# Kernel optimization log

Hardware: AMD Instinct MI355X
Metric: run time of the kernel (lower is better)

The kernel has to match this reference:

```python
import jax, jax.numpy as jnp
import numpy as np

BN_EPS = 1e-5


def setup_inputs() -> dict:
    key = jax.random.key(0)
    k1, k2, k3, k4 = jax.random.split(key, 4)
    N_IN, N_OUT, K, M, C_IN, C_OUT = 500000, 125000, 27, 60000, 64, 64
    x = jax.random.normal(k1, (N_IN, C_IN), dtype=jnp.float32)
    # Per-offset conv weights, fan-in scaled like Minkowski's kaiming init
    W = jax.random.normal(k2, (K, C_IN, C_OUT), dtype=jnp.float32) * (1.0 / np.sqrt(K * C_IN))
    gamma = jnp.ones((C_OUT,), dtype=jnp.float32)
    beta = jnp.zeros((C_OUT,), dtype=jnp.float32)
    # Kernel map: for each of the 27 offsets, M (input_idx, output_idx) pairs
    in_idx = jax.random.randint(k3, (K, M), 0, N_IN, dtype=jnp.int64)
    out_idx = jax.random.randint(k4, (K, M), 0, N_OUT, dtype=jnp.int64)
    return {"x": x, "W": W, "gamma": gamma, "beta": beta,
            "in_idx": in_idx, "out_idx": out_idx, "n_out": 125000}


def reference(x, W, gamma, beta, in_idx, out_idx, n_out):
    # Sparse 3D conv via kernel map: gather -> per-offset GEMM -> scatter-add.
    C_out = W.shape[-1]
    gathered = x[in_idx]                                   # [K, M, C_in]
    contrib = jnp.einsum('kmc,kcd->kmd', gathered, W)      # [K, M, C_out]
    out = jnp.zeros((n_out, C_out), dtype=x.dtype)
    out = out.at[out_idx.reshape(-1)].add(contrib.reshape(-1, C_out))  # [N_out, C_out]
    # MinkowskiBatchNorm (training mode): per-channel batch stats over all points
    mean = jnp.mean(out, axis=0)
    var = jnp.mean(jnp.square(out - mean), axis=0)         # biased variance
    y = (out - mean) * jax.lax.rsqrt(var + BN_EPS) * gamma + beta
    return y
```

## Files before the change

### kernel.cpp

```cpp
#include <hip/hip_runtime.h>

typedef __attribute__((ext_vector_type(8))) short short8;
typedef __attribute__((ext_vector_type(4))) float f32x4;

#define K_OFF    27
#define M_PAIRS  60000
#define C_DIM    64
#define N_IN     500000
#define N_OUT_C  125000
#define BN_EPS   1e-5f
#define E_TOT    (K_OFF * M_PAIRS)

#define TILE_ROWS    32
#define TILES_PER_K  (M_PAIRS / TILE_ROWS)
#define TOTAL_WT     (K_OFF * TILES_PER_K)

#define CONTRIB_BYTES ((size_t)E_TOT * C_DIM * 2)
#define WT_OFF    CONTRIB_BYTES
#define WT_BYTES  ((size_t)K_OFF * C_DIM * C_DIM * 2)
#define CNT_OFF   (WT_OFF + WT_BYTES)
#define CNT_BYTES ((size_t)N_OUT_C * 4)
#define OFF_OFF   (CNT_OFF + CNT_BYTES)
#define CUR_OFF   (OFF_OFF + CNT_BYTES)
#define BSUM_OFF  (CUR_OFF + CNT_BYTES)
#define ST_OFF    (BSUM_OFF + 4096)
#define XB_OFF    ((ST_OFF + 512 + 255) & ~(size_t)255)
#define XB_BYTES  ((size_t)N_IN * C_DIM * 2)
#define WS_MID    XB_OFF
#define WS_FULL   (XB_OFF + XB_BYTES)

#define SCAN_BS 256
#define SCAN_NB ((N_OUT_C + SCAN_BS - 1) / SCAN_BS)

#define PREP_XBLK 2048
#define PREP_WBLK ((K_OFF * C_DIM * C_DIM + 255) / 256)
#define PREP_HBLK 1024

__device__ __forceinline__ unsigned short f32_to_bf16(float f) {
    unsigned u = __float_as_uint(f);
    u += 0x7FFFu + ((u >> 16) & 1u);
    return (unsigned short)(u >> 16);
}
__device__ __forceinline__ float bf16f(unsigned short u) {
    return __uint_as_float((unsigned)u << 16);
}

__global__ __launch_bounds__(256) void prep(
    const float* __restrict__ x, unsigned short* __restrict__ xb,
    const float* __restrict__ W, unsigned short* __restrict__ wt,
    const int* __restrict__ out_idx, unsigned* __restrict__ cnt, int nx)
{
    int b = blockIdx.x;
    if (b < nx) {
        const int tid = b * 256 + threadIdx.x;
        const int T   = nx * 256;
        const int n4  = N_IN * C_DIM / 4;
        const float4* x4 = (const float4*)x;
        ushort4* b4 = (ushort4*)xb;
        for (int i = tid; i < n4; i += T) {
            float4 v = x4[i];
            ushort4 o;
            o.x = f32_to_bf16(v.x); o.y = f32_to_bf16(v.y);
            o.z = f32_to_bf16(v.z); o.w = f32_to_bf16(v.w);
            b4[i] = o;
        }
        return;
    }
    b -= nx;
    if (b < PREP_WBLK) {
        const int tid = b * 256 + threadIdx.x;
        if (tid < K_OFF * C_DIM * C_DIM) {
            const int c = tid & 63;
            const int d = (tid >> 6) & 63;
            const int k = tid >> 12;
            wt[tid] = f32_to_bf16(W[(k << 12) + (c << 6) + d]);
        }
        return;
    }
    b -= PREP_WBLK;
    for (int e = b * 256 + threadIdx.x; e < E_TOT; e += PREP_HBLK * 256)
        atomicAdd(&cnt[out_idx[e]], 1u);
}

__global__ __launch_bounds__(SCAN_BS) void scan_a(const unsigned* __restrict__ cnt,
                                                  unsigned* __restrict__ off,
                                                  unsigned* __restrict__ bsum) {
    __shared__ unsigned s[SCAN_BS];
    const int idx = blockIdx.x * SCAN_BS + threadIdx.x;
    const unsigned v = (idx < N_OUT_C) ? cnt[idx] : 0u;
    s[threadIdx.x] = v;
    __syncthreads();
    for (int d = 1; d < SCAN_BS; d <<= 1) {
        unsigned t = (threadIdx.x >= d) ? s[threadIdx.x - d] : 0u;
        __syncthreads();
        s[threadIdx.x] += t;
        __syncthreads();
    }
    if (idx < N_OUT_C) off[idx] = s[threadIdx.x] - v;
    if (threadIdx.x == SCAN_BS - 1) bsum[blockIdx.x] = s[threadIdx.x];
}

__global__ __launch_bounds__(512) void scan_b(unsigned* __restrict__ bsum) {
    __shared__ unsigned s[512];
    const unsigned v = (threadIdx.x < SCAN_NB) ? bsum[threadIdx.x] : 0u;
    s[threadIdx.x] = v;
    __syncthreads();
    for (int d = 1; d < 512; d <<= 1) {
        unsigned t = (threadIdx.x >= d) ? s[threadIdx.x - d] : 0u;
        __syncthreads();
        s[threadIdx.x] += t;
        __syncthreads();
    }
    if (threadIdx.x < SCAN_NB) bsum[threadIdx.x] = s[threadIdx.x] - v;
}

__global__ __launch_bounds__(SCAN_BS) void scan_c(unsigned* __restrict__ off,
                                                  unsigned* __restrict__ cur,
                                                  const unsigned* __restrict__ bsum) {
    const int idx = blockIdx.x * SCAN_BS + threadIdx.x;
    if (idx < N_OUT_C) {
        const unsigned o = off[idx] + bsum[blockIdx.x];
        off[idx] = o;
        cur[idx] = o;
    }
}

template<bool BF16G>
__global__ __launch_bounds__(256, 5) void mfma_contrib(
    const float* __restrict__ x, const unsigned short* __restrict__ xb,
    const unsigned short* __restrict__ wt,
    const int* __restrict__ in_idx, const int* __restrict__ out_idx,
    unsigned* __restrict__ cursor, unsigned short* __restrict__ contrib)
{
    const int gwave = blockIdx.x * 4 + (threadIdx.x >> 6);
    if (gwave >= TOTAL_WT) return;
    const int lane = threadIdx.x & 63;
    const int lg = lane >> 4;
    const int lr = lane & 15;

    const int k  = gwave / TILES_PER_K;
    const int t  = gwave % TILES_PER_K;
    const int m0 = t * TILE_ROWS;
    const int kbase = k * M_PAIRS;

    short8 bfr[2][4];
    const unsigned short* wtk = wt + (size_t)k * C_DIM * C_DIM;
#pragma unroll
    for (int ks = 0; ks < 2; ++ks)
#pragma unroll
        for (int ct = 0; ct < 4; ++ct)
            bfr[ks][ct] = *(const short8*)(wtk + (ct * 16 + lr) * C_DIM + ks * 32 + lg * 8);

    int pos = 0;
    if (lane < TILE_ROWS)
        pos = (int)atomicAdd(&cursor[out_idx[kbase + m0 + lane]], 1u);

    int aidx[2];
#pragma unroll
    for (int rt = 0; rt < 2; ++rt)
        aidx[rt] = in_idx[kbase + m0 + rt * 16 + lr];

    f32x4 acc[2][4] = {};
#pragma unroll
    for (int ks = 0; ks < 2; ++ks) {
#pragma unroll
        for (int rt = 0; rt < 2; ++rt) {
            short8 a;
            if constexpr (BF16G) {
                a = *(const short8*)(xb + (size_t)aidx[rt] * C_DIM + ks * 32 + lg * 8);
            } else {
                const float* xr = x + (size_t)aidx[rt] * C_DIM + ks * 32 + lg * 8;
                float4 f0 = *(const float4*)xr;
                float4 f1 = *(const float4*)(xr + 4);
                a[0] = (short)f32_to_bf16(f0.x); a[1] = (short)f32_to_bf16(f0.y);
                a[2] = (short)f32_to_bf16(f0.z); a[3] = (short)f32_to_bf16(f0.w);
                a[4] = (short)f32_to_bf16(f1.x); a[5] = (short)f32_to_bf16(f1.y);
                a[6] = (short)f32_to_bf16(f1.z); a[7] = (short)f32_to_bf16(f1.w);
            }
#pragma unroll
            for (int ct = 0; ct < 4; ++ct)
                acc[rt][ct] = __builtin_amdgcn_mfma_f32_16x16x32_bf16(
                    a, bfr[ks][ct], acc[rt][ct], 0, 0, 0);
        }
    }

#pragma unroll
    for (int rt = 0; rt < 2; ++rt) {
#pragma unroll
        for (int j = 0; j < 4; ++j) {
            const int r = rt * 16 + lg * 4 + j;
            const int p = __shfl(pos, r);
#pragma unroll
            for (int ct = 0; ct < 4; ++ct) {
                const float v0 = acc[rt][ct][j];
                const float v1 = __shfl_xor(v0, 1);
                if ((lane & 1) == 0) {
                    const unsigned pk = (unsigned)f32_to_bf16(v0)
                                      | ((unsigned)f32_to_bf16(v1) << 16);
                    *(unsigned*)(contrib + (size_t)p * C_DIM + ct * 16 + lr) = pk;
                }
            }
        }
    }
}

__global__ __launch_bounds__(256) void reduce_bn(
    const unsigned short* __restrict__ contrib, const unsigned* __restrict__ off,
    const unsigned* __restrict__ cnt, float* __restrict__ out,
    float* __restrict__ stats)
{
    __shared__ float ls[128];
    if (threadIdx.x < 128) ls[threadIdx.x] = 0.f;
    __syncthreads();
    const int lane = threadIdx.x & 63;
    const int wid  = blockIdx.x * 4 + (threadIdx.x >> 6);
    const int NW   = gridDim.x * 4;
    const int span = (N_OUT_C + NW - 1) / NW;
    const int o0 = wid * span;
    const int o1 = (o0 + span < N_OUT_C) ? o0 + span : N_OUT_C;

    float ssum = 0.f, ssq = 0.f;
    for (int o = o0; o < o1; ++o) {
        const unsigned base = off[o];
        const unsigned n    = cnt[o];
        const unsigned short* p = contrib + (size_t)base * C_DIM + lane;
        float a0 = 0.f, a1 = 0.f, a2 = 0.f, a3 = 0.f;
        unsigned i = 0;
        for (; i + 4 <= n; i += 4) {
            a0 += bf16f(p[(size_t)(i + 0) * C_DIM]);
            a1 += bf16f(p[(size_t)(i + 1) * C_DIM]);
            a2 += bf16f(p[(size_t)(i + 2) * C_DIM]);
            a3 += bf16f(p[(size_t)(i + 3) * C_DIM]);
        }
        for (; i < n; ++i) a0 += bf16f(p[(size_t)i * C_DIM]);
        const float acc = (a0 + a1) + (a2 + a3);
        out[(size_t)o * C_DIM + lane] = acc;
        ssum += acc;
        ssq = fmaf(acc, acc, ssq);
    }
    atomicAdd(&ls[lane], ssum);
    atomicAdd(&ls[64 + lane], ssq);
    __syncthreads();
    if (threadIdx.x < 128) unsafeAtomicAdd(&stats[threadIdx.x], ls[threadIdx.x]);
}

__global__ __launch_bounds__(256) void bn_apply_f32(
    float* __restrict__ out, const float* __restrict__ stats,
    const float* __restrict__ gamma, const float* __restrict__ beta)
{
    __shared__ float ssc[C_DIM], ssh[C_DIM];
    if (threadIdx.x < C_DIM) {
        const float inv_n = 1.0f / (float)N_OUT_C;
        float mean = stats[threadIdx.x] * inv_n;
        float var  = stats[C_DIM + threadIdx.x] * inv_n - mean * mean;
        float inv  = rsqrtf(var + BN_EPS);
        float s    = inv * gamma[threadIdx.x];
        ssc[threadIdx.x] = s;
        ssh[threadIdx.x] = beta[threadIdx.x] - mean * s;
    }
    __syncthreads();
    const int tid = blockIdx.x * blockDim.x + threadIdx.x;
    const int T   = gridDim.x * blockDim.x;
    const int cq  = (tid & 15) * 4;
    const int total4 = N_OUT_C * C_DIM / 4;
    const float4 sc = make_float4(ssc[cq], ssc[cq+1], ssc[cq+2], ssc[cq+3]);
    const float4 sh = make_float4(ssh[cq], ssh[cq+1], ssh[cq+2], ssh[cq+3]);
    float4* o4 = (float4*)out;
    for (int i = tid; i < total4; i += T) {
        float4 v = o4[i];
        v.x = fmaf(v.x, sc.x, sh.x);
        v.y = fmaf(v.y, sc.y, sh.y);
        v.z = fmaf(v.z, sc.z, sh.z);
        v.w = fmaf(v.w, sc.w, sh.w);
        o4[i] = v;
    }
}

#define FCHUNKS  37
#define FWPK     (FCHUNKS * 4)
#define FSPAN    ((M_PAIRS + FWPK - 1) / FWPK)

__global__ __launch_bounds__(256, 4) void conv_scatter(
    const float* __restrict__ x, const float* __restrict__ W,
    const int* __restrict__ in_idx, const int* __restrict__ out_idx,
    float* __restrict__ out)
{
    const int k     = blockIdx.x / FCHUNKS;
    const int chunk = blockIdx.x % FCHUNKS;
    const int wid   = chunk * 4 + (threadIdx.x >> 6);
    const int lane  = threadIdx.x & 63;
    float wcol[C_DIM];
    const float* Wk = W + (size_t)k * C_DIM * C_DIM;
#pragma unroll
    for (int c = 0; c < C_DIM; ++c) wcol[c] = Wk[c * C_DIM + lane];
    const int kbase = k * M_PAIRS;
    const int m0 = wid * FSPAN;
    const int m1 = (m0 + FSPAN < M_PAIRS) ? m0 + FSPAN : M_PAIRS;
    for (int m = m0; m < m1; ++m) {
        int ii = __builtin_amdgcn_readfirstlane(in_idx[kbase + m]);
        int oi = __builtin_amdgcn_readfirstlane(out_idx[kbase + m]);
        const float* xr = x + (size_t)ii * C_DIM;
        float a0=0.f,a1=0.f,a2=0.f,a3=0.f;
#pragma unroll
        for (int c = 0; c < C_DIM; c += 4) {
            a0 = fmaf(xr[c+0], wcol[c+0], a0);
            a1 = fmaf(xr[c+1], wcol[c+1], a1);
            a2 = fmaf(xr[c+2], wcol[c+2], a2);
            a3 = fmaf(xr[c+3], wcol[c+3], a3);
        }
        unsafeAtomicAdd(out + (size_t)oi * C_DIM + lane, (a0+a1)+(a2+a3));
    }
}

__global__ __launch_bounds__(256) void bn_stats_f32(
    const float* __restrict__ acc, float* __restrict__ stats)
{
    const int tid = blockIdx.x * blockDim.x + threadIdx.x;
    const int T   = gridDim.x * blockDim.x;
    const int cq  = (tid & 15) * 4;
    const int total4 = N_OUT_C * C_DIM / 4;
    float s0=0,s1=0,s2=0,s3=0,q0=0,q1=0,q2=0,q3=0;
    const float4* a4 = (const float4*)acc;
    for (int i = tid; i < total4; i += T) {
        float4 v = a4[i];
        s0+=v.x; q0=fmaf(v.x,v.x,q0);
        s1+=v.y; q1=fmaf(v.y,v.y,q1);
        s2+=v.z; q2=fmaf(v.z,v.z,q2);
        s3+=v.w; q3=fmaf(v.w,v.w,q3);
    }
    __shared__ float ls[128];
    if (threadIdx.x < 128) ls[threadIdx.x] = 0.f;
    __syncthreads();
    atomicAdd(&ls[cq+0],s0); atomicAdd(&ls[cq+1],s1);
    atomicAdd(&ls[cq+2],s2); atomicAdd(&ls[cq+3],s3);
    atomicAdd(&ls[64+cq+0],q0); atomicAdd(&ls[64+cq+1],q1);
    atomicAdd(&ls[64+cq+2],q2); atomicAdd(&ls[64+cq+3],q3);
    __syncthreads();
    if (threadIdx.x < 128) unsafeAtomicAdd(&stats[threadIdx.x], ls[threadIdx.x]);
}

extern "C" void kernel_launch(void* const* d_in, const int* in_sizes, int n_in,
                              void* d_out, int out_size, void* d_ws, size_t ws_size,
                              hipStream_t stream)
{
    const float* x       = (const float*)d_in[0];
    const float* W       = (const float*)d_in[1];
    const float* gamma   = (const float*)d_in[2];
    const float* beta    = (const float*)d_in[3];
    const int*   in_idx  = (const int*)d_in[4];
    const int*   out_idx = (const int*)d_in[5];
    float* out = (float*)d_out;

    if (ws_size >= WS_MID) {
        unsigned short* contrib = (unsigned short*)d_ws;
        unsigned short* wt      = (unsigned short*)((char*)d_ws + WT_OFF);
        unsigned* cnt           = (unsigned*)((char*)d_ws + CNT_OFF);
        unsigned* off           = (unsigned*)((char*)d_ws + OFF_OFF);
        unsigned* cur           = (unsigned*)((char*)d_ws + CUR_OFF);
        unsigned* bsum          = (unsigned*)((char*)d_ws + BSUM_OFF);
        float* stats            = (float*)((char*)d_ws + ST_OFF);
        unsigned short* xb      = (unsigned short*)((char*)d_ws + XB_OFF);
        const bool full         = (ws_size >= WS_FULL);
        const int nx            = full ? PREP_XBLK : 0;

        hipMemsetAsync(cnt, 0, CNT_BYTES, stream);
        hipMemsetAsync(stats, 0, 128 * sizeof(float), stream);
        prep<<<nx + PREP_WBLK + PREP_HBLK, 256, 0, stream>>>(
            x, xb, W, wt, out_idx, cnt, nx);
        scan_a<<<SCAN_NB, SCAN_BS, 0, stream>>>(cnt, off, bsum);
        scan_b<<<1, 512, 0, stream>>>(bsum);
        scan_c<<<SCAN_NB, SCAN_BS, 0, stream>>>(off, cur, bsum);
        if (full)
            mfma_contrib<true><<<(TOTAL_WT + 3) / 4, 256, 0, stream>>>(
                x, xb, wt, in_idx, out_idx, cur, contrib);
        else
            mfma_contrib<false><<<(TOTAL_WT + 3) / 4, 256, 0, stream>>>(
                x, xb, wt, in_idx, out_idx, cur, contrib);
        reduce_bn<<<2048, 256, 0, stream>>>(contrib, off, cnt, out, stats);
        bn_apply_f32<<<1024, 256, 0, stream>>>(out, stats, gamma, beta);
    } else {
        float* stats = (float*)d_ws;
        hipMemsetAsync(out, 0, (size_t)N_OUT_C * C_DIM * sizeof(float), stream);
        hipMemsetAsync(stats, 0, 128 * sizeof(float), stream);
        conv_scatter<<<K_OFF * FCHUNKS, 256, 0, stream>>>(x, W, in_idx, out_idx, out);
        bn_stats_f32<<<512, 256, 0, stream>>>(out, stats);
        bn_apply_f32<<<1024, 256, 0, stream>>>(out, stats, gamma, beta);
    }
}
```

Baseline: 402.1 us.

## Enlarge MFMA contrib tiles to 64 rows and vectorize reduce_bn row loads

```diff
diff --git a/kernel.cpp b/kernel.cpp
--- a/kernel.cpp
+++ b/kernel.cpp
@@ -11,8 +11,7 @@
 #define BN_EPS   1e-5f
 #define E_TOT    (K_OFF * M_PAIRS)
 
-#define TILE_ROWS    32
-#define TILES_PER_K  (M_PAIRS / TILE_ROWS)
+#define TILES_PER_K  ((M_PAIRS + 63) / 64)
 #define TOTAL_WT     (K_OFF * TILES_PER_K)
 
 #define CONTRIB_BYTES ((size_t)E_TOT * C_DIM * 2)
@@ -126,7 +125,7 @@
 }
 
 template<bool BF16G>
-__global__ __launch_bounds__(256, 5) void mfma_contrib(
+__global__ __launch_bounds__(256, 4) void mfma_contrib(
     const float* __restrict__ x, const unsigned short* __restrict__ xb,
     const unsigned short* __restrict__ wt,
     const int* __restrict__ in_idx, const int* __restrict__ out_idx,
@@ -140,7 +139,7 @@
 
     const int k  = gwave / TILES_PER_K;
     const int t  = gwave % TILES_PER_K;
-    const int m0 = t * TILE_ROWS;
+    const int m0 = t * 64;
     const int kbase = k * M_PAIRS;
 
     short8 bfr[2][4];
@@ -151,31 +150,38 @@
         for (int ct = 0; ct < 4; ++ct)
             bfr[ks][ct] = *(const short8*)(wtk + (ct * 16 + lr) * C_DIM + ks * 32 + lg * 8);
 
-    int pos = 0;
-    if (lane < TILE_ROWS)
-        pos = (int)atomicAdd(&cursor[out_idx[kbase + m0 + lane]], 1u);
-
-    int aidx[2];
-#pragma unroll
-    for (int rt = 0; rt < 2; ++rt)
-        aidx[rt] = in_idx[kbase + m0 + rt * 16 + lr];
-
-    f32x4 acc[2][4] = {};
+    int pos = -1;
+    {
+        const int mrow = m0 + lane;
+        if (mrow < M_PAIRS)
+            pos = (int)atomicAdd(&cursor[out_idx[kbase + mrow]], 1u);
+    }
+
+    int aidx[4];
+#pragma unroll
+    for (int rt = 0; rt < 4; ++rt) {
+        const int m = m0 + rt * 16 + lr;
+        aidx[rt] = (m < M_PAIRS) ? in_idx[kbase + m] : -1;
+    }
+
+    f32x4 acc[4][4] = {};
 #pragma unroll
     for (int ks = 0; ks < 2; ++ks) {
 #pragma unroll
-        for (int rt = 0; rt < 2; ++rt) {
-            short8 a;
-            if constexpr (BF16G) {
-                a = *(const short8*)(xb + (size_t)aidx[rt] * C_DIM + ks * 32 + lg * 8);
-            } else {
-                const float* xr = x + (size_t)aidx[rt] * C_DIM + ks * 32 + lg * 8;
-                float4 f0 = *(const float4*)xr;
-                float4 f1 = *(const float4*)(xr + 4);
-                a[0] = (short)f32_to_bf16(f0.x); a[1] = (short)f32_to_bf16(f0.y);
-                a[2] = (short)f32_to_bf16(f0.z); a[3] = (short)f32_to_bf16(f0.w);
-                a[4] = (short)f32_to_bf16(f1.x); a[5] = (short)f32_to_bf16(f1.y);
-                a[6] = (short)f32_to_bf16(f1.z); a[7] = (short)f32_to_bf16(f1.w);
+        for (int rt = 0; rt < 4; ++rt) {
+            short8 a = {};
+            if (aidx[rt] >= 0) {
+                if constexpr (BF16G) {
+                    a = *(const short8*)(xb + (size_t)aidx[rt] * C_DIM + ks * 32 + lg * 8);
+                } else {
+                    const float* xr = x + (size_t)aidx[rt] * C_DIM + ks * 32 + lg * 8;
+                    float4 f0 = *(const float4*)xr;
+                    float4 f1 = *(const float4*)(xr + 4);
+                    a[0] = (short)f32_to_bf16(f0.x); a[1] = (short)f32_to_bf16(f0.y);
+                    a[2] = (short)f32_to_bf16(f0.z); a[3] = (short)f32_to_bf16(f0.w);
+                    a[4] = (short)f32_to_bf16(f1.x); a[5] = (short)f32_to_bf16(f1.y);
+                    a[6] = (short)f32_to_bf16(f1.z); a[7] = (short)f32_to_bf16(f1.w);
+                }
             }
 #pragma unroll
             for (int ct = 0; ct < 4; ++ct)
@@ -185,20 +191,16 @@
     }
 
 #pragma unroll
-    for (int rt = 0; rt < 2; ++rt) {
+    for (int rt = 0; rt < 4; ++rt) {
 #pragma unroll
         for (int j = 0; j < 4; ++j) {
             const int r = rt * 16 + lg * 4 + j;
             const int p = __shfl(pos, r);
-#pragma unroll
-            for (int ct = 0; ct < 4; ++ct) {
-                const float v0 = acc[rt][ct][j];
-                const float v1 = __shfl_xor(v0, 1);
-                if ((lane & 1) == 0) {
-                    const unsigned pk = (unsigned)f32_to_bf16(v0)
-                                      | ((unsigned)f32_to_bf16(v1) << 16);
-                    *(unsigned*)(contrib + (size_t)p * C_DIM + ct * 16 + lr) = pk;
-                }
+            if (p >= 0) {
+                unsigned short* dst = contrib + (size_t)p * C_DIM + lr;
+#pragma unroll
+                for (int ct = 0; ct < 4; ++ct)
+                    dst[ct * 16] = f32_to_bf16(acc[rt][ct][j]);
             }
         }
     }
@@ -213,33 +215,45 @@
     if (threadIdx.x < 128) ls[threadIdx.x] = 0.f;
     __syncthreads();
     const int lane = threadIdx.x & 63;
+    const int lg = lane >> 4;
+    const int lr = lane & 15;
     const int wid  = blockIdx.x * 4 + (threadIdx.x >> 6);
     const int NW   = gridDim.x * 4;
     const int span = (N_OUT_C + NW - 1) / NW;
     const int o0 = wid * span;
     const int o1 = (o0 + span < N_OUT_C) ? o0 + span : N_OUT_C;
 
-    float ssum = 0.f, ssq = 0.f;
+    float ts0 = 0, ts1 = 0, ts2 = 0, ts3 = 0;
+    float tq0 = 0, tq1 = 0, tq2 = 0, tq3 = 0;
     for (int o = o0; o < o1; ++o) {
         const unsigned base = off[o];
-        const unsigned n    = cnt[o];
-        const unsigned short* p = contrib + (size_t)base * C_DIM + lane;
-        float a0 = 0.f, a1 = 0.f, a2 = 0.f, a3 = 0.f;
-        unsigned i = 0;
-        for (; i + 4 <= n; i += 4) {
-            a0 += bf16f(p[(size_t)(i + 0) * C_DIM]);
-            a1 += bf16f(p[(size_t)(i + 1) * C_DIM]);
-            a2 += bf16f(p[(size_t)(i + 2) * C_DIM]);
-            a3 += bf16f(p[(size_t)(i + 3) * C_DIM]);
-        }
-        for (; i < n; ++i) a0 += bf16f(p[(size_t)i * C_DIM]);
-        const float acc = (a0 + a1) + (a2 + a3);
-        out[(size_t)o * C_DIM + lane] = acc;
-        ssum += acc;
-        ssq = fmaf(acc, acc, ssq);
-    }
-    atomicAdd(&ls[lane], ssum);
-    atomicAdd(&ls[64 + lane], ssq);
+        const int n = (int)cnt[o];
+        float s0 = 0, s1 = 0, s2 = 0, s3 = 0;
+        for (int i = lg; i < n; i += 4) {
+            const ushort4 u = *(const ushort4*)(
+                contrib + ((size_t)base + i) * C_DIM + lr * 4);
+            s0 += bf16f(u.x); s1 += bf16f(u.y);
+            s2 += bf16f(u.z); s3 += bf16f(u.w);
+        }
+        s0 += __shfl_xor(s0, 16); s1 += __shfl_xor(s1, 16);
+        s2 += __shfl_xor(s2, 16); s3 += __shfl_xor(s3, 16);
+        s0 += __shfl_xor(s0, 32); s1 += __shfl_xor(s1, 32);
+        s2 += __shfl_xor(s2, 32); s3 += __shfl_xor(s3, 32);
+        if (lg == 0) {
+            *(float4*)(out + (size_t)o * C_DIM + lr * 4) =
+                make_float4(s0, s1, s2, s3);
+            ts0 += s0; tq0 = fmaf(s0, s0, tq0);
+            ts1 += s1; tq1 = fmaf(s1, s1, tq1);
+            ts2 += s2; tq2 = fmaf(s2, s2, tq2);
+            ts3 += s3; tq3 = fmaf(s3, s3, tq3);
+        }
+    }
+    if (lg == 0) {
+        atomicAdd(&ls[lr * 4 + 0], ts0); atomicAdd(&ls[lr * 4 + 1], ts1);
+        atomicAdd(&ls[lr * 4 + 2], ts2); atomicAdd(&ls[lr * 4 + 3], ts3);
+        atomicAdd(&ls[64 + lr * 4 + 0], tq0); atomicAdd(&ls[64 + lr * 4 + 1], tq1);
+        atomicAdd(&ls[64 + lr * 4 + 2], tq2); atomicAdd(&ls[64 + lr * 4 + 3], tq3);
+    }
     __syncthreads();
     if (threadIdx.x < 128) unsafeAtomicAdd(&stats[threadIdx.x], ls[threadIdx.x]);
 }
```

After: 394.3 us. About the same (-1.9%).
